# Performance work log

Hardware: AMD Instinct MI355X
Metric: run time of the kernel (lower is better)

## Reference

```python
import jax, jax.numpy as jnp
import numpy as np

# QTIP QuantizedLinear config (decode_mode='lut')
IN_F, OUT_F = 4096, 4096
TD_X, TD_Y = 16, 16          # weight tile
L, K, V = 16, 2, 2           # trellis state bits, bits/weight, values/state
TLUT_BITS = 16               # lut mode: tlut_bits == L


def fwht(x):
    """Normalized fast Walsh-Hadamard transform over the last axis (power of 2).
    Equivalent to matmul_hadU with K=1 (features are powers of two)."""
    n = x.shape[-1]
    h = 1
    while h < n:
        x = x.reshape(x.shape[:-1] + (n // (2 * h), 2, h))
        a, b = x[..., 0, :], x[..., 1, :]
        x = jnp.stack([a + b, a - b], axis=-2).reshape(x.shape[:-3] + (n,))
        h *= 2
    return x / jnp.sqrt(jnp.float32(n))


def dequantize_weight(trellis, tlut):
    """Bitshift trellis decode: each 16x16 tile stores td_x*td_y*K = 512 bits.
    The stream is walked KV = K*V bits per step (tail-biting); each L-bit state
    indexes the LUT producing V weights. trellis holds uint16 words in int32."""
    num_tiles = trellis.shape[0]
    T = TD_X * TD_Y            # 256 weights per tile
    S = T // V                 # 128 trellis steps per tile
    KV = K * V                 # 4 fresh bits per step
    steps = L // KV            # 4 nibbles form one L-bit state
    words = trellis & 0xFFFF
    bit_pos = jnp.arange(15, -1, -1)                     # MSB-first within word
    bits = (words[:, :, None] >> bit_pos) & 1            # (tiles, 32, 16)
    nib_w = 2 ** jnp.arange(KV - 1, -1, -1)
    nibs = jnp.sum(bits.reshape(num_tiles, S, KV) * nib_w, axis=-1)  # (tiles, S)
    # state_i = (nib[i-3]<<12)|(nib[i-2]<<8)|(nib[i-1]<<4)|nib[i], wraparound (tail-biting)
    states = jnp.zeros_like(nibs)
    for j in range(steps):
        states = states | (jnp.roll(nibs, j, axis=1) << (KV * j))
    vals = tlut[states]                                  # (tiles, S, V)
    W = vals.reshape(OUT_F // TD_X, IN_F // TD_Y, TD_X, TD_Y)
    return W.transpose(0, 2, 1, 3).reshape(OUT_F, IN_F)


def setup_inputs() -> dict:
    key = jax.random.key(0)
    k1, k2, k3, k4, k5 = jax.random.split(key, 5)
    inp = jax.random.normal(k1, (8, 2048, IN_F), jnp.float32)
    num_tiles = (OUT_F // TD_X) * (IN_F // TD_Y)
    words = (TD_X * TD_Y * K + 15) // 16
    trellis = jax.random.randint(k2, (num_tiles, words), 0, 65536, jnp.int32)
    tlut = jax.random.normal(k3, (2 ** TLUT_BITS, V), jnp.float32)
    SU = jax.random.normal(k4, (IN_F,), jnp.float32)
    SV = jax.random.normal(k5, (OUT_F,), jnp.float32)
    return {"input": inp, "trellis": trellis, "tlut": tlut, "SU": SU, "SV": SV}


def reference(input, trellis, tlut, SU, SV):
    W = dequantize_weight(trellis, tlut)          # (OUT_F, IN_F)
    x = input.reshape(-1, IN_F) * SU              # input rescale (sign vector)
    x = fwht(x)                                   # left Hadamard rotation
    x = x @ W.T                                   # fused dequant matmul
    x = fwht(x)                                   # right Hadamard rotation
    x = x * SV                                    # output rescale
    return x.reshape(input.shape[:-1] + (OUT_F,))
```

## Files before the change

kernel.cpp:

```cpp
#include <hip/hip_runtime.h>

typedef __attribute__((ext_vector_type(8))) short short8;
typedef __attribute__((ext_vector_type(4))) float f32x4;

__device__ __forceinline__ unsigned short f2bf(float f) {
  union { float f; unsigned u; } x{f};
  unsigned r = x.u + 0x7FFFu + ((x.u >> 16) & 1u);
  return (unsigned short)(r >> 16);
}

__device__ __forceinline__ void gload_lds16(const void* g, void* l) {
  __builtin_amdgcn_global_load_lds(
      (__attribute__((address_space(1))) void*)((unsigned long long)g),
      (__attribute__((address_space(3))) void*)(unsigned)((unsigned long long)l),
      16, 0, 0);
}

__device__ __forceinline__ void butterfly64(float (*tile)[64], int t) {
  const int c  = t & 63;
  const int pb = t >> 6;
#pragma unroll
  for (int h = 1; h < 64; h <<= 1) {
#pragma unroll
    for (int k = 0; k < 8; ++k) {
      const int p  = pb + (k << 2);
      const int j1 = ((p & ~(h - 1)) << 1) | (p & (h - 1));
      const int j2 = j1 + h;
      const float a = tile[j1][c], b = tile[j2][c];
      tile[j1][c] = a + b;
      tile[j2][c] = a - b;
    }
    __syncthreads();
  }
}

__global__ void k_deq_col1(const int* __restrict__ trellis,
                           const float* __restrict__ tlut,
                           float* __restrict__ W) {
  __shared__ unsigned short words[16][32];
  __shared__ float tile[64][64];
  const int t  = threadIdx.x;
  const int rg = blockIdx.x >> 6;
  const int cg = blockIdx.x & 63;
#pragma unroll
  for (int r = 0; r < 2; ++r) {
    const int ff = t + (r << 8);
    const int a = ff >> 7, rw = ff & 127;
    const int src = ((rg * 4 + a) * 256 + cg * 4) * 32 + rw;
    ((unsigned short*)words)[a * 128 + rw] = (unsigned short)(trellis[src] & 0xFFFF);
  }
  __syncthreads();
#pragma unroll
  for (int r = 0; r < 8; ++r) {
    const int f  = t + (r << 8);
    const int tl = f >> 7, s = f & 127;
    const unsigned short* w = words[tl];
    unsigned state = 0;
#pragma unroll
    for (int j = 0; j < 4; ++j) {
      const int ss = (s - j) & 127;
      state |= (((unsigned)w[ss >> 2] >> (12 - 4 * (ss & 3))) & 0xFu) << (4 * j);
    }
    const float2 v = *(const float2*)(tlut + (size_t)state * 2);
    const int o = ((tl >> 2) << 4) + (s >> 3);
    const int i = ((tl & 3) << 4) + ((s & 7) << 1);
    tile[o][i]     = v.x;
    tile[o][i + 1] = v.y;
  }
  __syncthreads();
  butterfly64(tile, t);
  const size_t base = ((size_t)(rg * 64)) * 4096 + cg * 64;
#pragma unroll
  for (int k = 0; k < 4; ++k) {
    const int idx = t + (k << 8);
    const int r = idx >> 4, c4 = idx & 15;
    *(float4*)(W + base + (size_t)r * 4096 + (c4 << 2)) = *(float4*)(&tile[r][c4 << 2]);
  }
}

__global__ void k_fwht_row(float* __restrict__ W) {
  __shared__ float row[4096];
  const int t = threadIdx.x;
  float* g = W + ((size_t)blockIdx.x << 12);
#pragma unroll
  for (int k = 0; k < 4; ++k) {
    const int e = (t + (k << 8)) << 2;
    *(float4*)(row + e) = *(const float4*)(g + e);
  }
  __syncthreads();
  for (int h = 1; h < 4096; h <<= 1) {
#pragma unroll
    for (int k = 0; k < 8; ++k) {
      const int p  = t + (k << 8);
      const int j1 = ((p & ~(h - 1)) << 1) | (p & (h - 1));
      const int j2 = j1 + h;
      const float a = row[j1], b = row[j2];
      row[j1] = a + b;
      row[j2] = a - b;
    }
    __syncthreads();
  }
#pragma unroll
  for (int k = 0; k < 4; ++k) {
    const int e = (t + (k << 8)) << 2;
    float4 v = *(float4*)(row + e);
    v.x *= 0.015625f; v.y *= 0.015625f; v.z *= 0.015625f; v.w *= 0.015625f;
    *(float4*)(g + e) = v;
  }
}

__global__ void k_fwht_col2(const float* __restrict__ W,
                            const float* __restrict__ SU,
                            const float* __restrict__ SV,
                            unsigned short* __restrict__ Mt) {
  __shared__ float tile[64][64];
  const int t  = threadIdx.x;
  const int b  = blockIdx.x >> 6;
  const int cg = blockIdx.x & 63;
#pragma unroll
  for (int k = 0; k < 4; ++k) {
    const int idx = t + (k << 8);
    const int a = idx >> 4, c4 = idx & 15;
    const int row = (a << 6) + b;
    *(float4*)(&tile[a][c4 << 2]) =
        *(const float4*)(W + (size_t)row * 4096 + ((size_t)cg << 6) + (c4 << 2));
  }
  __syncthreads();
  butterfly64(tile, t);
#pragma unroll
  for (int k = 0; k < 4; ++k) {
    const int idx = t + (k << 8);
    const int a = idx >> 4, c4 = idx & 15;
    const int row = (a << 6) + b;
    const int col0 = (cg << 6) + (c4 << 2);
    const float sv = SV[row] * 0.015625f;
    const float4 su = *(const float4*)(SU + col0);
    const float4 v = *(float4*)(&tile[a][c4 << 2]);
    ushort4 o;
    o.x = f2bf(v.x * sv * su.x);
    o.y = f2bf(v.y * sv * su.y);
    o.z = f2bf(v.z * sv * su.z);
    o.w = f2bf(v.w * sv * su.w);
    *(ushort4*)(Mt + (size_t)row * 4096 + col0) = o;
  }
}

__global__ void k_cvt_x(const float* __restrict__ x, unsigned short* __restrict__ xb) {
  const long long n4 = (long long)16384 * 4096 / 4;
  long long i = (long long)blockIdx.x * blockDim.x + threadIdx.x;
  const long long stride = (long long)gridDim.x * blockDim.x;
  for (; i < n4; i += stride) {
    const float4 v = *(const float4*)(x + i * 4);
    ushort4 o;
    o.x = f2bf(v.x); o.y = f2bf(v.y); o.z = f2bf(v.z); o.w = f2bf(v.w);
    *(ushort4*)(xb + i * 4) = o;
  }
}

#define BARRIER __builtin_amdgcn_s_barrier()
#define WAITV0  asm volatile("s_waitcnt vmcnt(0)" ::: "memory")

#define STAGE_A(db, jj) do { \
  gload_lds16(aRow,                      smem +         (db)*32768 +         w1k + ((size_t)(jj) << 6)*2); \
  gload_lds16(aRow + ( 64ull << 12),     smem +         (db)*32768 +  8192 + w1k + ((size_t)(jj) << 6)*2); \
  gload_lds16(aRow + (128ull << 12),     smem +         (db)*32768 + 16384 + w1k + ((size_t)(jj) << 6)*2); \
  gload_lds16(aRow + (192ull << 12),     smem +         (db)*32768 + 24576 + w1k + ((size_t)(jj) << 6)*2); \
} while (0)
#define STAGE_B(db, jj) do { \
  gload_lds16(bRow,                      smem + 65536 + (db)*32768 +         w1k + ((size_t)(jj) << 6)*2); \
  gload_lds16(bRow + ( 64ull << 12),     smem + 65536 + (db)*32768 +  8192 + w1k + ((size_t)(jj) << 6)*2); \
  gload_lds16(bRow + (128ull << 12),     smem + 65536 + (db)*32768 + 16384 + w1k + ((size_t)(jj) << 6)*2); \
  gload_lds16(bRow + (192ull << 12),     smem + 65536 + (db)*32768 + 24576 + w1k + ((size_t)(jj) << 6)*2); \
} while (0)

#define RD_AF(kk, base, cx) do { _Pragma("unroll") \
  for (int mi = 0; mi < 8; ++mi) af[mi][kk] = *(const short8*)((base) + mi*2048 + (cx)); } while (0)
#define RD_BB(kk, base, cx) do { _Pragma("unroll") \
  for (int ni = 0; ni < 4; ++ni) bb[ni][kk] = *(const short8*)((base) + ni*2048 + (cx)); } while (0)

#define MMA_K(kk) do { _Pragma("unroll") \
  for (int mi = 0; mi < 8; ++mi) { \
    acc[mi][0] = __builtin_amdgcn_mfma_f32_16x16x32_bf16(af[mi][kk], bb[0][kk], acc[mi][0], 0, 0, 0); \
    acc[mi][1] = __builtin_amdgcn_mfma_f32_16x16x32_bf16(af[mi][kk], bb[1][kk], acc[mi][1], 0, 0, 0); \
    acc[mi][2] = __builtin_amdgcn_mfma_f32_16x16x32_bf16(af[mi][kk], bb[2][kk], acc[mi][2], 0, 0, 0); \
    acc[mi][3] = __builtin_amdgcn_mfma_f32_16x16x32_bf16(af[mi][kk], bb[3][kk], acc[mi][3], 0, 0, 0); \
  } } while (0)

#define KTILE(Asx, Bsx, STAGES) do { \
  WAITV0; BARRIER; \
  STAGES; \
  RD_BB(0, Bsx, cx0); RD_AF(0, Asx, cx0); \
  __builtin_amdgcn_s_setprio(1); MMA_K(0); __builtin_amdgcn_s_setprio(0); \
  RD_BB(1, Bsx, cx1); RD_AF(1, Asx, cx1); \
  __builtin_amdgcn_s_setprio(1); MMA_K(1); __builtin_amdgcn_s_setprio(0); \
} while (0)

#define STAGE_ALL(db, jj) do { \
  const unsigned short* aJ = aRow + ((jj) << 6); \
  const unsigned short* bJ = bRow + ((jj) << 6); \
  gload_lds16(aJ,                  smem +         (db)*32768 +         w1k); \
  gload_lds16(aJ + ( 64ull << 12), smem +         (db)*32768 +  8192 + w1k); \
  gload_lds16(aJ + (128ull << 12), smem +         (db)*32768 + 16384 + w1k); \
  gload_lds16(aJ + (192ull << 12), smem +         (db)*32768 + 24576 + w1k); \
  gload_lds16(bJ,                  smem + 65536 + (db)*32768 +         w1k); \
  gload_lds16(bJ + ( 64ull << 12), smem + 65536 + (db)*32768 +  8192 + w1k); \
  gload_lds16(bJ + (128ull << 12), smem + 65536 + (db)*32768 + 16384 + w1k); \
  gload_lds16(bJ + (192ull << 12), smem + 65536 + (db)*32768 + 24576 + w1k); \
} while (0)

__global__ void __launch_bounds__(512, 2)
k_gemm8(const unsigned short* __restrict__ A,
        const unsigned short* __restrict__ B,
        float* __restrict__ C) {
  extern __shared__ char smem[];
  const int t    = threadIdx.x;
  const int lane = t & 63, w = t >> 6;
  const int wr   = w >> 2, wc = w & 3;
  const int hb   = wc >> 1, rb = (wc & 1) * 64;
  const int lr   = lane & 15, q = lane >> 4;
  const int w1k  = w * 1024;

  const int nt = blockIdx.x & 15;
  const int mt = blockIdx.x >> 4;

  const int cx0 = lr * 128 + (((0 + q) ^ (lr & 7)) << 4);
  const int cx1 = lr * 128 + (((4 + q) ^ (lr & 7)) << 4);

  const char* As0 = smem +         wr * 16384;
  const char* As1 = smem + 32768 + wr * 16384;
  const char* Bs0 = smem + 65536 +         hb * 16384 + rb * 128;
  const char* Bs1 = smem + 65536 + 32768 + hb * 16384 + rb * 128;

  const int srow  = t >> 3;
  const int csrc8 = (((t & 7) ^ (srow & 7)) << 3);
  const unsigned short* aRow = A + (((size_t)(mt * 256 + srow)) << 12) + csrc8;
  const unsigned short* bRow = B + (((size_t)(nt * 256 + srow)) << 12) + csrc8;

  short8 af[8][2], bb[4][2];
  f32x4  acc[8][4];
#pragma unroll
  for (int i = 0; i < 8; ++i)
#pragma unroll
    for (int j = 0; j < 4; ++j) acc[i][j] = (f32x4){0.f, 0.f, 0.f, 0.f};

  STAGE_ALL(0, 0);

  for (int g = 0; g < 31; ++g) {
    KTILE(As0, Bs0, STAGE_ALL(1, 2 * g + 1));
    KTILE(As1, Bs1, STAGE_ALL(0, 2 * g + 2));
  }
  KTILE(As0, Bs0, STAGE_ALL(1, 63));
  KTILE(As1, Bs1, {});

  float* cbase = C + (((size_t)(mt * 256 + wr * 128 + q * 4)) << 12)
               + nt * 256 + wc * 64 + lr;
#pragma unroll
  for (int mi = 0; mi < 8; ++mi)
#pragma unroll
    for (int ni = 0; ni < 4; ++ni)
#pragma unroll
      for (int r = 0; r < 4; ++r)
        cbase[(((size_t)(mi * 16 + r)) << 12) + ni * 16] = acc[mi][ni][r];
}

extern "C" void kernel_launch(void* const* d_in, const int* in_sizes, int n_in,
                              void* d_out, int out_size, void* d_ws, size_t ws_size,
                              hipStream_t stream) {
  const float* x       = (const float*)d_in[0];
  const int*   trellis = (const int*)d_in[1];
  const float* tlut    = (const float*)d_in[2];
  const float* SU      = (const float*)d_in[3];
  const float* SV      = (const float*)d_in[4];
  float* out = (float*)d_out;

  char* ws = (char*)d_ws;
  float*          W  = (float*)ws;
  unsigned short* Mt = (unsigned short*)(ws + (64ull << 20));
  unsigned short* xb = (unsigned short*)(ws + (96ull << 20));

  hipFuncSetAttribute(reinterpret_cast<const void*>(&k_gemm8),
                      hipFuncAttributeMaxDynamicSharedMemorySize, 131072);

  hipLaunchKernelGGL(k_deq_col1,  dim3(4096),  dim3(256), 0, stream, trellis, tlut, W);
  hipLaunchKernelGGL(k_fwht_row,  dim3(4096),  dim3(256), 0, stream, W);
  hipLaunchKernelGGL(k_fwht_col2, dim3(4096),  dim3(256), 0, stream, W, SU, SV, Mt);
  hipLaunchKernelGGL(k_cvt_x,     dim3(2048),  dim3(256), 0, stream, x, xb);
  hipLaunchKernelGGL(k_gemm8,     dim3(1024),  dim3(512), 131072, stream, xb, Mt, out);
}
```

Measured before the change: 622.2 us.

## Stream A fragments per MFMA row and remap block IDs across XCDs

The GEMM inner loop no longer preloads all eight A fragments and four B fragments for both k-halves. It loads B once per half and streams A fragments one ahead of the MFMAs, which cuts VGPR pressure and interleaves LDS reads with matrix ops. The block index is also permuted so that consecutive hardware block IDs, which are dealt round-robin across the 8 XCDs, map to contiguous tiles within each XCD for better L2 reuse. Less register prefetch depth may expose LDS latency between MFMAs.

```diff
diff --git a/kernel.cpp b/kernel.cpp
--- a/kernel.cpp
+++ b/kernel.cpp
@@ -160,41 +160,6 @@
 #define BARRIER __builtin_amdgcn_s_barrier()
 #define WAITV0  asm volatile("s_waitcnt vmcnt(0)" ::: "memory")
 
-#define STAGE_A(db, jj) do { \
-  gload_lds16(aRow,                      smem +         (db)*32768 +         w1k + ((size_t)(jj) << 6)*2); \
-  gload_lds16(aRow + ( 64ull << 12),     smem +         (db)*32768 +  8192 + w1k + ((size_t)(jj) << 6)*2); \
-  gload_lds16(aRow + (128ull << 12),     smem +         (db)*32768 + 16384 + w1k + ((size_t)(jj) << 6)*2); \
-  gload_lds16(aRow + (192ull << 12),     smem +         (db)*32768 + 24576 + w1k + ((size_t)(jj) << 6)*2); \
-} while (0)
-#define STAGE_B(db, jj) do { \
-  gload_lds16(bRow,                      smem + 65536 + (db)*32768 +         w1k + ((size_t)(jj) << 6)*2); \
-  gload_lds16(bRow + ( 64ull << 12),     smem + 65536 + (db)*32768 +  8192 + w1k + ((size_t)(jj) << 6)*2); \
-  gload_lds16(bRow + (128ull << 12),     smem + 65536 + (db)*32768 + 16384 + w1k + ((size_t)(jj) << 6)*2); \
-  gload_lds16(bRow + (192ull << 12),     smem + 65536 + (db)*32768 + 24576 + w1k + ((size_t)(jj) << 6)*2); \
-} while (0)
-
-#define RD_AF(kk, base, cx) do { _Pragma("unroll") \
-  for (int mi = 0; mi < 8; ++mi) af[mi][kk] = *(const short8*)((base) + mi*2048 + (cx)); } while (0)
-#define RD_BB(kk, base, cx) do { _Pragma("unroll") \
-  for (int ni = 0; ni < 4; ++ni) bb[ni][kk] = *(const short8*)((base) + ni*2048 + (cx)); } while (0)
-
-#define MMA_K(kk) do { _Pragma("unroll") \
-  for (int mi = 0; mi < 8; ++mi) { \
-    acc[mi][0] = __builtin_amdgcn_mfma_f32_16x16x32_bf16(af[mi][kk], bb[0][kk], acc[mi][0], 0, 0, 0); \
-    acc[mi][1] = __builtin_amdgcn_mfma_f32_16x16x32_bf16(af[mi][kk], bb[1][kk], acc[mi][1], 0, 0, 0); \
-    acc[mi][2] = __builtin_amdgcn_mfma_f32_16x16x32_bf16(af[mi][kk], bb[2][kk], acc[mi][2], 0, 0, 0); \
-    acc[mi][3] = __builtin_amdgcn_mfma_f32_16x16x32_bf16(af[mi][kk], bb[3][kk], acc[mi][3], 0, 0, 0); \
-  } } while (0)
-
-#define KTILE(Asx, Bsx, STAGES) do { \
-  WAITV0; BARRIER; \
-  STAGES; \
-  RD_BB(0, Bsx, cx0); RD_AF(0, Asx, cx0); \
-  __builtin_amdgcn_s_setprio(1); MMA_K(0); __builtin_amdgcn_s_setprio(0); \
-  RD_BB(1, Bsx, cx1); RD_AF(1, Asx, cx1); \
-  __builtin_amdgcn_s_setprio(1); MMA_K(1); __builtin_amdgcn_s_setprio(0); \
-} while (0)
-
 #define STAGE_ALL(db, jj) do { \
   const unsigned short* aJ = aRow + ((jj) << 6); \
   const unsigned short* bJ = bRow + ((jj) << 6); \
@@ -208,6 +173,31 @@
   gload_lds16(bJ + (192ull << 12), smem + 65536 + (db)*32768 + 24576 + w1k); \
 } while (0)
 
+#define HALF_K(Asx, Bsx, cx) do { \
+  bb[0] = *(const short8*)((Bsx) + 0*2048 + (cx)); \
+  bb[1] = *(const short8*)((Bsx) + 1*2048 + (cx)); \
+  bb[2] = *(const short8*)((Bsx) + 2*2048 + (cx)); \
+  bb[3] = *(const short8*)((Bsx) + 3*2048 + (cx)); \
+  short8 acur = *(const short8*)((Asx) + 0*2048 + (cx)); \
+  _Pragma("unroll") \
+  for (int mi = 0; mi < 8; ++mi) { \
+    short8 anxt = acur; \
+    if (mi < 7) anxt = *(const short8*)((Asx) + (mi + 1) * 2048 + (cx)); \
+    acc[mi][0] = __builtin_amdgcn_mfma_f32_16x16x32_bf16(acur, bb[0], acc[mi][0], 0, 0, 0); \
+    acc[mi][1] = __builtin_amdgcn_mfma_f32_16x16x32_bf16(acur, bb[1], acc[mi][1], 0, 0, 0); \
+    acc[mi][2] = __builtin_amdgcn_mfma_f32_16x16x32_bf16(acur, bb[2], acc[mi][2], 0, 0, 0); \
+    acc[mi][3] = __builtin_amdgcn_mfma_f32_16x16x32_bf16(acur, bb[3], acc[mi][3], 0, 0, 0); \
+    acur = anxt; \
+  } \
+} while (0)
+
+#define KTILE(Asx, Bsx, STAGES) do { \
+  WAITV0; BARRIER; \
+  STAGES; \
+  HALF_K(Asx, Bsx, cx0); \
+  HALF_K(Asx, Bsx, cx1); \
+} while (0)
+
 __global__ void __launch_bounds__(512, 2)
 k_gemm8(const unsigned short* __restrict__ A,
         const unsigned short* __restrict__ B,
@@ -220,8 +210,9 @@
   const int lr   = lane & 15, q = lane >> 4;
   const int w1k  = w * 1024;
 
-  const int nt = blockIdx.x & 15;
-  const int mt = blockIdx.x >> 4;
+  const int bid = ((blockIdx.x & 7) << 7) + (blockIdx.x >> 3);
+  const int nt  = bid & 15;
+  const int mt  = bid >> 4;
 
   const int cx0 = lr * 128 + (((0 + q) ^ (lr & 7)) << 4);
   const int cx1 = lr * 128 + (((4 + q) ^ (lr & 7)) << 4);
@@ -236,7 +227,7 @@
   const unsigned short* aRow = A + (((size_t)(mt * 256 + srow)) << 12) + csrc8;
   const unsigned short* bRow = B + (((size_t)(nt * 256 + srow)) << 12) + csrc8;
 
-  short8 af[8][2], bb[4][2];
+  short8 bb[4];
   f32x4  acc[8][4];
 #pragma unroll
   for (int i = 0; i < 8; ++i)
```

After: 691.5 us. 11.1% more time.
